# Performance work log

Hardware: AMD Instinct MI355X
Metric: run time of the kernel (lower is better)

The kernel has to match this reference:

```python
import jax, jax.numpy as jnp
import numpy as np

BETA = 0.001       # gamma of the soft-min
THRESHOLD = 2.0    # padding cost for 'skip' slots


def _build_cost(centers_a, centers_b):
    # sort by timestamp (last column), then drop it (keep_times=False)
    a = centers_a[jnp.argsort(centers_a[:, -1])][:, :-1]
    b = centers_b[jnp.argsort(centers_b[:, -1])][:, :-1]
    a = a / jnp.sqrt(jnp.sum(a * a, axis=-1, keepdims=True) + 1e-10)
    b = b / jnp.sqrt(jnp.sum(b * b, axis=-1, keepdims=True) + 1e-10)
    cost = 1.0 - a @ b.T                      # [M, N] cosine cost
    M, N = cost.shape
    # interleave real costs with threshold 'skip' columns: [M, 2N]
    c2 = jnp.concatenate([cost, jnp.full_like(cost, THRESHOLD)], axis=0)  # [2M, N]
    c3 = c2.T.reshape(2 * N, M).T                                         # [M, 2N]
    c4 = jnp.concatenate(
        [jnp.full((M, 1), THRESHOLD, dtype=cost.dtype), c3], axis=1)      # [M, 2N+1]
    return jax.nn.softmax(c4, axis=-1)  # softmax='row'


def _dwsa_loss(C, gamma):
    # C: [M, K] with K = 2N+1. DP: D[i,j] = softmin(D[i-1, :p_j]) + C[i,j]
    # where p_j = j+1 for even j, j for odd j (prefix soft-min of previous row).
    M, K = C.shape
    j = jnp.arange(K)
    idx = jnp.where(j % 2 == 0, j, j - 1)  # inclusive prefix end index

    def step(d_prev, c_row):
        # stable prefix soft-min via cumulative logsumexp of -D/gamma
        lcse = jax.lax.cumlogsumexp(-d_prev / gamma)   # [K]
        softmin = -gamma * lcse[idx]                   # [K]
        d = softmin + c_row
        return d, None

    d_last, _ = jax.lax.scan(step, C[0], C[1:])
    # final soft-min over last row
    return -gamma * jax.nn.logsumexp(-d_last / gamma)


def setup_inputs() -> dict:
    key = jax.random.key(0)
    k1, k2 = jax.random.split(key)
    centers_a = jax.random.normal(k1, (2048, 513), dtype=jnp.float32)
    centers_b = jax.random.normal(k2, (2048, 513), dtype=jnp.float32)
    return {"centers_a": centers_a, "centers_b": centers_b}


def reference(centers_a, centers_b):
    C = _build_cost(centers_a, centers_b)
    return _dwsa_loss(C, BETA)
```

## Files before the change

### kernel.cpp

```cpp
#include <hip/hip_runtime.h>
#include <math.h>

#define M_ROWS 2048
#define N_COLS 2048
#define DIMS 512
#define IN_STRIDE 513
#define DP_BLOCKS 32
#define DP_COLS 64
#define BAND 16

constexpr float GAMMA = 0.001f;
constexpr float LOG2E = 1.44269504088896f;
constexpr float LN2   = 0.69314718055995f;

__device__ __forceinline__ float fexp2(float x) { return __builtin_amdgcn_exp2f(x); }
__device__ __forceinline__ float flog2(float x) { return __builtin_amdgcn_logf(x); }

__global__ void argsort_kernel(const float* __restrict__ a, const float* __restrict__ b,
                               int* __restrict__ permA, int* __restrict__ permB) {
    const float* src = blockIdx.y ? b : a;
    int* perm = blockIdx.y ? permB : permA;
    __shared__ float keys[M_ROWS];
    for (int j = threadIdx.x; j < M_ROWS; j += blockDim.x)
        keys[j] = src[(size_t)j * IN_STRIDE + DIMS];
    __syncthreads();
    int i = blockIdx.x * blockDim.x + threadIdx.x;
    float ki = keys[i];
    int rank = 0;
    for (int j = 0; j < M_ROWS; ++j) {
        float kj = keys[j];
        rank += (kj < ki) || (kj == ki && j < i);
    }
    perm[rank] = i;
}

__global__ __launch_bounds__(128) void norm_kernel(const float* __restrict__ a, const float* __restrict__ b,
                                                   const int* __restrict__ permA, const int* __restrict__ permB,
                                                   float* __restrict__ Ahat, float* __restrict__ Bhat) {
    const float* src = blockIdx.y ? b : a;
    const int* perm = blockIdx.y ? permB : permA;
    float* dst = blockIdx.y ? Bhat : Ahat;
    int r = blockIdx.x;
    int row = perm[r];
    const float* p = src + (size_t)row * IN_STRIDE;
    int tid = threadIdx.x;
    float v0 = p[tid], v1 = p[tid + 128], v2 = p[tid + 256], v3 = p[tid + 384];
    float ss = v0 * v0 + v1 * v1 + v2 * v2 + v3 * v3;
    #pragma unroll
    for (int off = 32; off > 0; off >>= 1) ss += __shfl_down(ss, off);
    __shared__ float red[2];
    if ((tid & 63) == 0) red[tid >> 6] = ss;
    __syncthreads();
    float inv = 1.0f / sqrtf(red[0] + red[1] + 1e-10f);
    float* q = dst + (size_t)r * DIMS;
    q[tid] = v0 * inv; q[tid + 128] = v1 * inv; q[tid + 256] = v2 * inv; q[tid + 384] = v3 * inv;
}

__global__ __launch_bounds__(256) void gemm_kernel(const float* __restrict__ A, const float* __restrict__ B,
                                                   float* __restrict__ Q) {
    __shared__ float As[16][68];
    __shared__ float Bs[16][68];
    int tid = threadIdx.x;
    int tx = tid & 15, ty = tid >> 4;
    int row0 = blockIdx.y * 64;
    int col0 = blockIdx.x * 64;
    int lrow = tid >> 2;
    int lk = (tid & 3) * 4;
    const float* ap = A + (size_t)(row0 + lrow) * DIMS + lk;
    const float* bp = B + (size_t)(col0 + lrow) * DIMS + lk;
    float acc[4][4] = {};
    for (int k0 = 0; k0 < DIMS; k0 += 16) {
        float4 av = *(const float4*)ap; ap += 16;
        float4 bv = *(const float4*)bp; bp += 16;
        __syncthreads();
        As[lk + 0][lrow] = av.x; As[lk + 1][lrow] = av.y; As[lk + 2][lrow] = av.z; As[lk + 3][lrow] = av.w;
        Bs[lk + 0][lrow] = bv.x; Bs[lk + 1][lrow] = bv.y; Bs[lk + 2][lrow] = bv.z; Bs[lk + 3][lrow] = bv.w;
        __syncthreads();
        #pragma unroll
        for (int k = 0; k < 16; ++k) {
            float4 a4 = *(const float4*)&As[k][ty * 4];
            float4 b4 = *(const float4*)&Bs[k][tx * 4];
            float aa[4] = {a4.x, a4.y, a4.z, a4.w};
            float bb[4] = {b4.x, b4.y, b4.z, b4.w};
            #pragma unroll
            for (int u = 0; u < 4; ++u)
                #pragma unroll
                for (int v = 0; v < 4; ++v)
                    acc[u][v] += aa[u] * bb[v];
        }
    }
    #pragma unroll
    for (int u = 0; u < 4; ++u) {
        float4 o;
        o.x = __expf(-1.0f - acc[u][0]);
        o.y = __expf(-1.0f - acc[u][1]);
        o.z = __expf(-1.0f - acc[u][2]);
        o.w = __expf(-1.0f - acc[u][3]);
        *(float4*)&Q[(size_t)(row0 + ty * 4 + u) * N_COLS + col0 + tx * 4] = o;
    }
}

__global__ __launch_bounds__(256) void rowstat_kernel(const float* __restrict__ Q,
                                                      float* __restrict__ rowscale,
                                                      float* __restrict__ ews) {
    int i = blockIdx.x;
    const float* q = Q + (size_t)i * N_COLS;
    int tid = threadIdx.x;
    float4 x = *(const float4*)(q + tid * 4);
    float4 y = *(const float4*)(q + 1024 + tid * 4);
    float s = x.x + x.y + x.z + x.w + y.x + y.y + y.z + y.w;
    #pragma unroll
    for (int off = 32; off > 0; off >>= 1) s += __shfl_down(s, off);
    __shared__ float red[4];
    if ((tid & 63) == 0) red[tid >> 6] = s;
    __syncthreads();
    if (tid == 0) {
        float denom = 2049.0f + red[0] + red[1] + red[2] + red[3];
        float rs = (LOG2E / GAMMA) / denom;
        rowscale[i] = rs;
        ews[i] = fexp2(-rs);
    }
}

__global__ __launch_bounds__(256) void lgt_kernel(const float* __restrict__ Q,
                                                  const float* __restrict__ rowscale,
                                                  float* __restrict__ ELT) {
    __shared__ float tile[64][65];
    const int row0 = blockIdx.y * 64;
    const int col0 = blockIdx.x * 64;
    const int t = threadIdx.x;
    const int c4 = (t & 15) * 4;
    const int r  = t >> 4;
    #pragma unroll
    for (int rr = 0; rr < 64; rr += 16) {
        int row = row0 + rr + r;
        float rs = rowscale[row];
        float4 v = *(const float4*)(Q + (size_t)row * N_COLS + col0 + c4);
        float e = fexp2(-rs);
        tile[c4 + 0][rr + r] = e + fexp2(-rs * v.x);
        tile[c4 + 1][rr + r] = e + fexp2(-rs * v.y);
        tile[c4 + 2][rr + r] = e + fexp2(-rs * v.z);
        tile[c4 + 3][rr + r] = e + fexp2(-rs * v.w);
    }
    __syncthreads();
    #pragma unroll
    for (int cc = 0; cc < 64; cc += 16) {
        int col = cc + r;
        float4 o;
        o.x = tile[col][c4 + 0];
        o.y = tile[col][c4 + 1];
        o.z = tile[col][c4 + 2];
        o.w = tile[col][c4 + 3];
        *(float4*)(ELT + (size_t)(col0 + col) * M_ROWS + row0 + c4) = o;
    }
}

#define KEEP4(v) asm volatile("" : "+v"(v.x), "+v"(v.y), "+v"(v.z), "+v"(v.w))

#define SST(V, MODS) asm("s_nop 1\n\tv_add_f32_dpp %0, %0, %0 " MODS : "+v"(V))
#define SCAN6                                                            \
    SST(t, "row_shr:1 row_mask:0xf bank_mask:0xf bound_ctrl:0");         \
    SST(t, "row_shr:2 row_mask:0xf bank_mask:0xf bound_ctrl:0");         \
    SST(t, "row_shr:4 row_mask:0xf bank_mask:0xf bound_ctrl:0");         \
    SST(t, "row_shr:8 row_mask:0xf bank_mask:0xf bound_ctrl:0");         \
    SST(t, "row_bcast:15 row_mask:0xa bank_mask:0xf bound_ctrl:0");      \
    SST(t, "row_bcast:31 row_mask:0xc bank_mask:0xf bound_ctrl:0")

#define DP_ROW(U, ELV, EWV, VCI)                                                 \
    {                                                                            \
        float ci = 0.f;                                                          \
        if (s > 0)                                                               \
            ci = __int_as_float(__builtin_amdgcn_readlane(                       \
                     __float_as_int(VCI), (U)));                                 \
        float t = w * (ELV);                                                     \
        float pre = fmaf(w, (EWV) - (ELV), ci);                                  \
        SCAN6;                                                                   \
        float all = ci + t;                                                      \
        float wn = pre + t;                                                      \
        if (s < DP_BLOCKS - 1) {                                                 \
            if (lane == 63) {                                                    \
                unsigned long long po =                                          \
                    ((unsigned long long)__float_as_uint(all) << 32)             \
                    | (unsigned long long)__float_as_uint(Rm);                   \
                __hip_atomic_store(pub + base + (U), po, __ATOMIC_RELAXED,       \
                                   __HIP_MEMORY_SCOPE_AGENT);                    \
            }                                                                    \
        } else {                                                                 \
            h = fmaf(h, (EWV), all);                                             \
        }                                                                        \
        w = wn;                                                                  \
    }

#define RENORM8                                                                  \
    {                                                                            \
        int e48 = __builtin_amdgcn_readlane(__builtin_amdgcn_frexp_expf(w), 48); \
        float f = __int_as_float((127 - e48) << 23);                             \
        w *= f; h *= f;                                                          \
        Rm += (float)e48;                                                        \
    }

#define WAIT_BAND                                                                \
    if (s > 0) {                                                                 \
        for (;;) {                                                               \
            unsigned long long miss = __ballot((lane < BAND) && pk == 0ull);     \
            if (miss == 0ull) break;                                             \
            if (pk == 0ull && lane < BAND)                                       \
                pk = __hip_atomic_load(sub + base + lane, __ATOMIC_RELAXED,      \
                                       __HIP_MEMORY_SCOPE_AGENT);               \
        }                                                                        \
        pkLo = (int)(unsigned)(pk & 0xFFFFFFFFull);                              \
        pkHi = (int)(unsigned)(pk >> 32);                                        \
    }

__global__ __launch_bounds__(64) void dp_kernel(const float* __restrict__ ELT,
                                                const float* __restrict__ Ews,
                                                unsigned long long* __restrict__ carry,
                                                float* __restrict__ out) {
    const int s = ((blockIdx.x & 7) << 2) | (blockIdx.x >> 3);
    const int lane = threadIdx.x;
    const float* lcol = ELT + (size_t)(s * DP_COLS + lane) * M_ROWS;
    unsigned long long* pub = carry + (size_t)s * M_ROWS;
    const unsigned long long* sub = carry + (size_t)(s - 1) * M_ROWS;

    float w = 1.f;
    float Rm = 0.f;
    float h = 1.f;

    float4 lq0 = *(const float4*)(lcol + 0);
    float4 lq1 = *(const float4*)(lcol + 4);
    float4 lq2 = *(const float4*)(lcol + 8);
    float4 lq3 = *(const float4*)(lcol + 12);
    float4 ev0 = *(const float4*)(Ews + 0);
    float4 ev1 = *(const float4*)(Ews + 4);
    float4 ev2 = *(const float4*)(Ews + 8);
    float4 ev3 = *(const float4*)(Ews + 12);
    KEEP4(lq0); KEEP4(lq1); KEEP4(lq2); KEEP4(lq3);
    KEEP4(ev0); KEEP4(ev1); KEEP4(ev2); KEEP4(ev3);

    unsigned long long pk = 1ull;
    if (s > 0 && lane < BAND)
        pk = __hip_atomic_load(sub + lane, __ATOMIC_RELAXED, __HIP_MEMORY_SCOPE_AGENT);

    for (int base = 0; base < M_ROWS; base += BAND) {
        float4 nl0{}, nl1{}, nl2{}, nl3{}, nv0{}, nv1{}, nv2{}, nv3{};
        if (base + BAND < M_ROWS) {
            nl0 = *(const float4*)(lcol + base + BAND);
            nl1 = *(const float4*)(lcol + base + BAND + 4);
            nl2 = *(const float4*)(lcol + base + BAND + 8);
            nl3 = *(const float4*)(lcol + base + BAND + 12);
            nv0 = *(const float4*)(Ews + base + BAND);
            nv1 = *(const float4*)(Ews + base + BAND + 4);
            nv2 = *(const float4*)(Ews + base + BAND + 8);
            nv3 = *(const float4*)(Ews + base + BAND + 12);
        }
        KEEP4(nl0); KEEP4(nl1); KEEP4(nl2); KEEP4(nl3);
        KEEP4(nv0); KEEP4(nv1); KEEP4(nv2); KEEP4(nv3);

        int pkLo = 0, pkHi = 0;
        WAIT_BAND
        float vci01 = 0.f;
        if (s > 0)
            vci01 = __int_as_float(pkHi) * fexp2(
                __int_as_float(__builtin_amdgcn_readlane(pkLo, 0)) - Rm);

        DP_ROW(0,  lq0.x, ev0.x, vci01)
        DP_ROW(1,  lq0.y, ev0.y, vci01)
        DP_ROW(2,  lq0.z, ev0.z, vci01)
        DP_ROW(3,  lq0.w, ev0.w, vci01)
        DP_ROW(4,  lq1.x, ev1.x, vci01)
        DP_ROW(5,  lq1.y, ev1.y, vci01)
        DP_ROW(6,  lq1.z, ev1.z, vci01)
        DP_ROW(7,  lq1.w, ev1.w, vci01)
        RENORM8
        float vci23 = 0.f;
        if (s > 0)
            vci23 = __int_as_float(pkHi) * fexp2(
                __int_as_float(__builtin_amdgcn_readlane(pkLo, 8)) - Rm);
        unsigned long long nk = 1ull;
        if (s > 0 && lane < BAND && base + BAND < M_ROWS)
            nk = __hip_atomic_load(sub + base + BAND + lane,
                                   __ATOMIC_RELAXED, __HIP_MEMORY_SCOPE_AGENT);

        DP_ROW(8,  lq2.x, ev2.x, vci23)
        DP_ROW(9,  lq2.y, ev2.y, vci23)
        DP_ROW(10, lq2.z, ev2.z, vci23)
        DP_ROW(11, lq2.w, ev2.w, vci23)
        DP_ROW(12, lq3.x, ev3.x, vci23)
        DP_ROW(13, lq3.y, ev3.y, vci23)
        DP_ROW(14, lq3.z, ev3.z, vci23)
        DP_ROW(15, lq3.w, ev3.w, vci23)
        RENORM8
        pk = nk;

        lq0 = nl0; lq1 = nl1; lq2 = nl2; lq3 = nl3;
        ev0 = nv0; ev1 = nv1; ev2 = nv2; ev3 = nv3;
    }
    if (s == DP_BLOCKS - 1 && lane == 63)
        out[0] = -GAMMA * LN2 * (Rm + flog2(h));
}

extern "C" void kernel_launch(void* const* d_in, const int* in_sizes, int n_in,
                              void* d_out, int out_size, void* d_ws, size_t ws_size,
                              hipStream_t stream) {
    (void)in_sizes; (void)n_in; (void)out_size; (void)ws_size;
    const float* a = (const float*)d_in[0];
    const float* b = (const float*)d_in[1];
    float* out = (float*)d_out;
    char* ws = (char*)d_ws;
    float* Q        = (float*)(ws);
    float* ELT      = (float*)(ws + (size_t)16 * 1024 * 1024);
    float* Ahat     = (float*)(ws + (size_t)32 * 1024 * 1024);
    float* Bhat     = (float*)(ws + (size_t)36 * 1024 * 1024);
    float* rowscale = (float*)(ws + (size_t)40 * 1024 * 1024);
    int* permA      = (int*)(ws + (size_t)40 * 1024 * 1024 + 8192);
    int* permB      = (int*)(ws + (size_t)40 * 1024 * 1024 + 16384);
    float* ews      = (float*)(ws + (size_t)40 * 1024 * 1024 + 24576);
    unsigned long long* carry = (unsigned long long*)(ws + (size_t)41 * 1024 * 1024);

    hipMemsetAsync(carry, 0, (size_t)DP_BLOCKS * M_ROWS * sizeof(unsigned long long), stream);
    argsort_kernel<<<dim3(8, 2), 256, 0, stream>>>(a, b, permA, permB);
    norm_kernel<<<dim3(2048, 2), 128, 0, stream>>>(a, b, permA, permB, Ahat, Bhat);
    gemm_kernel<<<dim3(32, 32), 256, 0, stream>>>(Ahat, Bhat, Q);
    rowstat_kernel<<<2048, 256, 0, stream>>>(Q, rowscale, ews);
    lgt_kernel<<<dim3(32, 32), 256, 0, stream>>>(Q, rowscale, ELT);
    dp_kernel<<<DP_BLOCKS, DP_COLS, 0, stream>>>(ELT, ews, carry, out);
}
```

Baseline: 579.1 us.

## Compute cosine GEMM with split-bf16 MFMA (hi/lo, three products)

The normalize kernel now writes each unit vector as a bf16 high part plus a bf16 residual low part. The FP32 SIMT GEMM is replaced by a matrix-core kernel using mfma_f32_16x16x32_bf16, running three products (lo*hi, hi*lo, hi*hi) to approximate FP32 accuracy. Operands are loaded straight from global memory with no LDS staging. This trades scalar FMA throughput for matrix instructions, at the cost of some precision loss and uncoalesced scalar output stores.

```diff
diff --git a/kernel.cpp b/kernel.cpp
--- a/kernel.cpp
+++ b/kernel.cpp
@@ -15,6 +15,14 @@
 
 __device__ __forceinline__ float fexp2(float x) { return __builtin_amdgcn_exp2f(x); }
 __device__ __forceinline__ float flog2(float x) { return __builtin_amdgcn_logf(x); }
+
+__device__ __forceinline__ unsigned short f2bf(float x) {
+    unsigned u = __float_as_uint(x);
+    return (unsigned short)((u + 0x7FFFu + ((u >> 16) & 1u)) >> 16);
+}
+__device__ __forceinline__ float bf2f(unsigned short u) {
+    return __uint_as_float((unsigned)u << 16);
+}
 
 __global__ void argsort_kernel(const float* __restrict__ a, const float* __restrict__ b,
                                int* __restrict__ permA, int* __restrict__ permB) {
@@ -36,10 +44,12 @@
 
 __global__ __launch_bounds__(128) void norm_kernel(const float* __restrict__ a, const float* __restrict__ b,
                                                    const int* __restrict__ permA, const int* __restrict__ permB,
-                                                   float* __restrict__ Ahat, float* __restrict__ Bhat) {
+                                                   unsigned short* __restrict__ Ahi, unsigned short* __restrict__ Alo,
+                                                   unsigned short* __restrict__ Bhi, unsigned short* __restrict__ Blo) {
     const float* src = blockIdx.y ? b : a;
     const int* perm = blockIdx.y ? permB : permA;
-    float* dst = blockIdx.y ? Bhat : Ahat;
+    unsigned short* dhi = blockIdx.y ? Bhi : Ahi;
+    unsigned short* dlo = blockIdx.y ? Blo : Alo;
     int r = blockIdx.x;
     int row = perm[r];
     const float* p = src + (size_t)row * IN_STRIDE;
@@ -52,51 +62,65 @@
     if ((tid & 63) == 0) red[tid >> 6] = ss;
     __syncthreads();
     float inv = 1.0f / sqrtf(red[0] + red[1] + 1e-10f);
-    float* q = dst + (size_t)r * DIMS;
-    q[tid] = v0 * inv; q[tid + 128] = v1 * inv; q[tid + 256] = v2 * inv; q[tid + 384] = v3 * inv;
-}
-
-__global__ __launch_bounds__(256) void gemm_kernel(const float* __restrict__ A, const float* __restrict__ B,
+    unsigned short* qh = dhi + (size_t)r * DIMS;
+    unsigned short* ql = dlo + (size_t)r * DIMS;
+    float x;
+    unsigned short h;
+    x = v0 * inv; h = f2bf(x); qh[tid]       = h; ql[tid]       = f2bf(x - bf2f(h));
+    x = v1 * inv; h = f2bf(x); qh[tid + 128] = h; ql[tid + 128] = f2bf(x - bf2f(h));
+    x = v2 * inv; h = f2bf(x); qh[tid + 256] = h; ql[tid + 256] = f2bf(x - bf2f(h));
+    x = v3 * inv; h = f2bf(x); qh[tid + 384] = h; ql[tid + 384] = f2bf(x - bf2f(h));
+}
+
+typedef __attribute__((ext_vector_type(8))) short bf16x8;
+typedef __attribute__((ext_vector_type(4))) float f32x4;
+
+__global__ __launch_bounds__(256) void gemm_kernel(const unsigned short* __restrict__ Ahi,
+                                                   const unsigned short* __restrict__ Alo,
+                                                   const unsigned short* __restrict__ Bhi,
+                                                   const unsigned short* __restrict__ Blo,
                                                    float* __restrict__ Q) {
-    __shared__ float As[16][68];
-    __shared__ float Bs[16][68];
-    int tid = threadIdx.x;
-    int tx = tid & 15, ty = tid >> 4;
-    int row0 = blockIdx.y * 64;
-    int col0 = blockIdx.x * 64;
-    int lrow = tid >> 2;
-    int lk = (tid & 3) * 4;
-    const float* ap = A + (size_t)(row0 + lrow) * DIMS + lk;
-    const float* bp = B + (size_t)(col0 + lrow) * DIMS + lk;
-    float acc[4][4] = {};
-    for (int k0 = 0; k0 < DIMS; k0 += 16) {
-        float4 av = *(const float4*)ap; ap += 16;
-        float4 bv = *(const float4*)bp; bp += 16;
-        __syncthreads();
-        As[lk + 0][lrow] = av.x; As[lk + 1][lrow] = av.y; As[lk + 2][lrow] = av.z; As[lk + 3][lrow] = av.w;
-        Bs[lk + 0][lrow] = bv.x; Bs[lk + 1][lrow] = bv.y; Bs[lk + 2][lrow] = bv.z; Bs[lk + 3][lrow] = bv.w;
-        __syncthreads();
-        #pragma unroll
-        for (int k = 0; k < 16; ++k) {
-            float4 a4 = *(const float4*)&As[k][ty * 4];
-            float4 b4 = *(const float4*)&Bs[k][tx * 4];
-            float aa[4] = {a4.x, a4.y, a4.z, a4.w};
-            float bb[4] = {b4.x, b4.y, b4.z, b4.w};
-            #pragma unroll
-            for (int u = 0; u < 4; ++u)
-                #pragma unroll
-                for (int v = 0; v < 4; ++v)
-                    acc[u][v] += aa[u] * bb[v];
-        }
-    }
-    #pragma unroll
-    for (int u = 0; u < 4; ++u) {
-        float4 o;
-        o.x = __expf(-1.0f - acc[u][0]);
-        o.y = __expf(-1.0f - acc[u][1]);
-        o.z = __expf(-1.0f - acc[u][2]);
-        o.w = __expf(-1.0f - acc[u][3]);
-        *(float4*)&Q[(size_t)(row0 + ty * 4 + u) * N_COLS + col0 + tx * 4] = o;
+    const int tid = threadIdx.x;
+    const int lane = tid & 63;
+    const int wv = tid >> 6;
+    const int row0 = blockIdx.y * 64 + (wv >> 1) * 32;
+    const int col0 = blockIdx.x * 64 + (wv & 1) * 32;
+    const int lr = lane & 15;
+    const int kj = (lane >> 4) * 8;
+    const size_t ar0 = (size_t)(row0 + lr) * DIMS + kj;
+    const size_t ar1 = (size_t)(row0 + 16 + lr) * DIMS + kj;
+    const size_t br0 = (size_t)(col0 + lr) * DIMS + kj;
+    const size_t br1 = (size_t)(col0 + 16 + lr) * DIMS + kj;
+    f32x4 acc00 = {}, acc01 = {}, acc10 = {}, acc11 = {};
+    for (int k0 = 0; k0 < DIMS; k0 += 32) {
+        bf16x8 a0h = *(const bf16x8*)(Ahi + ar0 + k0);
+        bf16x8 a1h = *(const bf16x8*)(Ahi + ar1 + k0);
+        bf16x8 a0l = *(const bf16x8*)(Alo + ar0 + k0);
+        bf16x8 a1l = *(const bf16x8*)(Alo + ar1 + k0);
+        bf16x8 b0h = *(const bf16x8*)(Bhi + br0 + k0);
+        bf16x8 b1h = *(const bf16x8*)(Bhi + br1 + k0);
+        bf16x8 b0l = *(const bf16x8*)(Blo + br0 + k0);
+        bf16x8 b1l = *(const bf16x8*)(Blo + br1 + k0);
+        acc00 = __builtin_amdgcn_mfma_f32_16x16x32_bf16(a0l, b0h, acc00, 0, 0, 0);
+        acc00 = __builtin_amdgcn_mfma_f32_16x16x32_bf16(a0h, b0l, acc00, 0, 0, 0);
+        acc00 = __builtin_amdgcn_mfma_f32_16x16x32_bf16(a0h, b0h, acc00, 0, 0, 0);
+        acc01 = __builtin_amdgcn_mfma_f32_16x16x32_bf16(a0l, b1h, acc01, 0, 0, 0);
+        acc01 = __builtin_amdgcn_mfma_f32_16x16x32_bf16(a0h, b1l, acc01, 0, 0, 0);
+        acc01 = __builtin_amdgcn_mfma_f32_16x16x32_bf16(a0h, b1h, acc01, 0, 0, 0);
+        acc10 = __builtin_amdgcn_mfma_f32_16x16x32_bf16(a1l, b0h, acc10, 0, 0, 0);
+        acc10 = __builtin_amdgcn_mfma_f32_16x16x32_bf16(a1h, b0l, acc10, 0, 0, 0);
+        acc10 = __builtin_amdgcn_mfma_f32_16x16x32_bf16(a1h, b0h, acc10, 0, 0, 0);
+        acc11 = __builtin_amdgcn_mfma_f32_16x16x32_bf16(a1l, b1h, acc11, 0, 0, 0);
+        acc11 = __builtin_amdgcn_mfma_f32_16x16x32_bf16(a1h, b1l, acc11, 0, 0, 0);
+        acc11 = __builtin_amdgcn_mfma_f32_16x16x32_bf16(a1h, b1h, acc11, 0, 0, 0);
+    }
+    const int rbase = (lane >> 4) * 4;
+    #pragma unroll
+    for (int r = 0; r < 4; ++r) {
+        Q[(size_t)(row0 + rbase + r) * N_COLS + col0 + lr]           = __expf(-1.0f - acc00[r]);
+        Q[(size_t)(row0 + rbase + r) * N_COLS + col0 + 16 + lr]      = __expf(-1.0f - acc01[r]);
+        Q[(size_t)(row0 + 16 + rbase + r) * N_COLS + col0 + lr]      = __expf(-1.0f - acc10[r]);
+        Q[(size_t)(row0 + 16 + rbase + r) * N_COLS + col0 + 16 + lr] = __expf(-1.0f - acc11[r]);
     }
 }
 
@@ -309,8 +333,10 @@
     char* ws = (char*)d_ws;
     float* Q        = (float*)(ws);
     float* ELT      = (float*)(ws + (size_t)16 * 1024 * 1024);
-    float* Ahat     = (float*)(ws + (size_t)32 * 1024 * 1024);
-    float* Bhat     = (float*)(ws + (size_t)36 * 1024 * 1024);
+    unsigned short* Ahi = (unsigned short*)(ws + (size_t)32 * 1024 * 1024);
+    unsigned short* Alo = (unsigned short*)(ws + (size_t)34 * 1024 * 1024);
+    unsigned short* Bhi = (unsigned short*)(ws + (size_t)36 * 1024 * 1024);
+    unsigned short* Blo = (unsigned short*)(ws + (size_t)38 * 1024 * 1024);
     float* rowscale = (float*)(ws + (size_t)40 * 1024 * 1024);
     int* permA      = (int*)(ws + (size_t)40 * 1024 * 1024 + 8192);
     int* permB      = (int*)(ws + (size_t)40 * 1024 * 1024 + 16384);
@@ -319,8 +345,8 @@
 
     hipMemsetAsync(carry, 0, (size_t)DP_BLOCKS * M_ROWS * sizeof(unsigned long long), stream);
     argsort_kernel<<<dim3(8, 2), 256, 0, stream>>>(a, b, permA, permB);
-    norm_kernel<<<dim3(2048, 2), 128, 0, stream>>>(a, b, permA, permB, Ahat, Bhat);
-    gemm_kernel<<<dim3(32, 32), 256, 0, stream>>>(Ahat, Bhat, Q);
+    norm_kernel<<<dim3(2048, 2), 128, 0, stream>>>(a, b, permA, permB, Ahi, Alo, Bhi, Blo);
+    gemm_kernel<<<dim3(32, 32), 256, 0, stream>>>(Ahi, Alo, Bhi, Blo, Q);
     rowstat_kernel<<<2048, 256, 0, stream>>>(Q, rowscale, ews);
     lgt_kernel<<<dim3(32, 32), 256, 0, stream>>>(Q, rowscale, ELT);
     dp_kernel<<<DP_BLOCKS, DP_COLS, 0, stream>>>(ELT, ews, carry, out);
```

New measurement: 582.4 us. Within noise of the previous version (+0.6%).
